# Performance work log

Hardware: AMD Instinct MI355X
Metric: run time of the kernel (lower is better)

Reference implementation:

```python
import jax, jax.numpy as jnp
import numpy as np

B, S, T = 32, 128, 64
V, E, H = 32000, 256, 512


def setup_inputs() -> dict:
    key = jax.random.key(0)
    ks = jax.random.split(key, 32)
    n = jax.random.normal

    def lin(k, fi, fo):
        kw, kb = jax.random.split(k)
        s = 1.0 / np.sqrt(fi)
        return (jax.random.uniform(kw, (fi, fo), jnp.float32, -s, s),
                jax.random.uniform(kb, (fo,), jnp.float32, -s, s))

    W_enc, b_enc = lin(ks[4], 2 * H, H)      # attention.enc_h_in
    W_prev, b_prev = lin(ks[5], H, H)        # attention.prev_s_in
    W_att, b_att = lin(ks[6], H, 1)          # attention.linear
    Wi_g, bi_g = lin(ks[7], E, 2 * H)        # cell.input_weights
    Wh_g, bh_g = lin(ks[8], H, 2 * H)        # cell.hidden_weights
    Wc_g, bc_g = lin(ks[9], 2 * H, 2 * H)    # cell.ctx_weights
    Wi, bi = lin(ks[10], E, H)               # cell.input_in
    Wh, bh = lin(ks[11], H, H)               # cell.hidden_in
    Wc, bc = lin(ks[12], 2 * H, H)           # cell.ctx_in
    W_out, b_out = lin(ks[13], H, V)         # dec2word

    return dict(
        content=n(ks[0], (B, H), jnp.float32),
        sentiment=n(ks[1], (B, H), jnp.float32),
        hiddens=n(ks[2], (B, S, 2 * H), jnp.float32),
        target=jax.random.randint(ks[3], (B, T), 0, V, jnp.int32),
        embed=n(ks[14], (V, E), jnp.float32) * 0.02,
        W_enc=W_enc, b_enc=b_enc, W_prev=W_prev, b_prev=b_prev,
        W_att=W_att, b_att=b_att,
        Wi_g=Wi_g, bi_g=bi_g, Wh_g=Wh_g, bh_g=bh_g, Wc_g=Wc_g, bc_g=bc_g,
        Wi=Wi, bi=bi, Wh=Wh, bh=bh, Wc=Wc, bc=bc,
        W_out=W_out, b_out=b_out,
    )


def reference(content, sentiment, hiddens, target, embed,
              W_enc, b_enc, W_prev, b_prev, W_att, b_att,
              Wi_g, bi_g, Wh_g, bh_g, Wc_g, bc_g,
              Wi, bi, Wh, bh, Wc, bc, W_out, b_out):
    tgt_emb = embed[target]                       # [B, T, E]
    enc_proj = hiddens @ W_enc + b_enc            # [B, S, H], timestep-invariant

    def step(prev_s, x_t):
        # additive attention
        q = prev_s @ W_prev + b_prev              # [B, H]
        h = jnp.tanh(enc_proj + q[:, None, :])    # [B, S, H]
        score = h @ W_att + b_att                 # [B, S, 1]
        alpha = jax.nn.softmax(score, axis=1)     # over source positions
        ctx = jnp.einsum('bsi,bsh->bh', alpha, hiddens)  # [B, 2H]
        # GRU-like cell (original uses only the first gate, as written)
        gates = x_t @ Wi_g + bi_g + prev_s @ Wh_g + bh_g + ctx @ Wc_g + bc_g
        reset_gate, _update_gate = jnp.split(gates, 2, axis=1)
        r = jax.nn.sigmoid(reset_gate)
        s_tilde = jnp.tanh(x_t @ Wi + bi + prev_s @ Wh + bh + ctx @ Wc + bc)
        new_s = (1.0 - r) * prev_s + r * s_tilde
        return new_s, new_s

    _, dec_h = jax.lax.scan(step, content, jnp.swapaxes(tgt_emb, 0, 1))
    dec_h = jnp.swapaxes(dec_h, 0, 1)             # [B, T, H]
    style_logits = sentiment @ W_out + b_out      # [B, V], same every step
    outputs = (dec_h @ W_out + b_out) + 0.5 * style_logits[:, None, :]
    return outputs                                # [B, T, V]
```

## Files before the change

kernel.cpp:

```cpp
#include <hip/hip_runtime.h>
#include <hip/hip_bf16.h>
#include <math.h>

#define NB 32
#define NS 128
#define NT 64
#define NV 32000
#define NE 256
#define NH 512

typedef short s16x8 __attribute__((ext_vector_type(8)));
typedef float f32x4 __attribute__((ext_vector_type(4)));
typedef unsigned u32x4 __attribute__((ext_vector_type(4)));

__device__ __forceinline__ unsigned short f2bf(float x) {
    union { float f; unsigned u; } v; v.f = x;
    unsigned r = v.u + 0x7FFFu + ((v.u >> 16) & 1u);
    return (unsigned short)(r >> 16);
}
__device__ __forceinline__ float bf2f(short h) {
    union { unsigned u; float f; } x;
    x.u = ((unsigned)(unsigned short)h) << 16;
    return x.f;
}

__device__ __forceinline__ void st_coh_b32(void* p, unsigned v) {
    asm volatile("global_store_dword %0, %1, off sc0 sc1" :: "v"(p), "v"(v) : "memory");
}
__device__ __forceinline__ unsigned ld_coh_b32(const void* p) {
    unsigned v;
    asm volatile("global_load_dword %0, %1, off sc0 sc1\n\ts_waitcnt vmcnt(0)"
                 : "=v"(v) : "v"(p) : "memory");
    return v;
}
__device__ __forceinline__ void ld_coh_2x128(const void* p0, const void* p1, u32x4& a, u32x4& b) {
    asm volatile("global_load_dwordx4 %0, %2, off sc0 sc1\n\t"
                 "global_load_dwordx4 %1, %3, off sc0 sc1\n\t"
                 "s_waitcnt vmcnt(0)"
                 : "=&v"(a), "=&v"(b) : "v"(p0), "v"(p1) : "memory");
}
__device__ __forceinline__ void ld_coh_3x32(const void* p0, const void* p1, const void* p2,
                                            float& a, float& b, float& c) {
    asm volatile("global_load_dword %0, %3, off sc0 sc1\n\t"
                 "global_load_dword %1, %4, off sc0 sc1\n\t"
                 "global_load_dword %2, %5, off sc0 sc1\n\t"
                 "s_waitcnt vmcnt(0)"
                 : "=&v"(a), "=&v"(b), "=&v"(c) : "v"(p0), "v"(p1), "v"(p2) : "memory");
}

__device__ __forceinline__ void wait_flags(const unsigned* flags, unsigned seq) {
    const int lane = threadIdx.x & 63;
    for (;;) {
        unsigned v = 0xFFFFFFFFu;
        if (lane < 32) v = ld_coh_b32(&flags[lane]);
        if (__all(v >= seq)) break;
    }
    asm volatile("" ::: "memory");
}

__global__ void build_wfrag_k(const float* __restrict__ Wp,
                              const float* __restrict__ Whg,
                              const float* __restrict__ Wh,
                              unsigned short* __restrict__ wfrag) {
    int blk = blockIdx.x;
    int lane = threadIdx.x;
    int ct = blk >> 4, kt = blk & 15;
    int c = ct * 16 + (lane & 15);
    int kb = kt * 32 + (lane >> 4) * 8;
    s16x8 v;
#pragma unroll
    for (int j = 0; j < 8; ++j) {
        int k = kb + j;
        float x;
        if (c < 512)       x = Wp[k * 512 + c];
        else if (c < 1024) x = Whg[k * 1024 + (c - 512)];
        else               x = Wh[k * 512 + (c - 1024)];
        v[j] = (short)f2bf(x);
    }
    ((s16x8*)wfrag)[blk * 64 + lane] = v;
}

template<int MODE>
__global__ __launch_bounds__(256, 2) void gemm_mfma(
    const float* __restrict__ Af, const unsigned short* __restrict__ Abf,
    const int* __restrict__ gidx,
    const float* __restrict__ B0, const float* __restrict__ B1, const float* __restrict__ B2,
    const float* __restrict__ e0, const float* __restrict__ e1, const float* __restrict__ e2,
    const float* __restrict__ e3, const float* __restrict__ e4, const float* __restrict__ e5,
    void* __restrict__ O0v, void* __restrict__ O1v, void* __restrict__ O2v)
{
    constexpr int M   = (MODE == 0) ? 4096 : 2048;
    constexpr int K   = (MODE == 0) ? 1024 : ((MODE == 1) ? 256 : 512);
    constexpr int LDA = (MODE == 0) ? 1024 : ((MODE == 1) ? 256 : 512);
    constexpr int MB  = M / 128;

    const int bm = blockIdx.x % MB, bn = blockIdx.x / MB;
    const int m0 = bm * 128, n0 = bn * 128;

    const float* Bp; int ldb, coff;
    if constexpr (MODE == 0) {
        int sub = n0 >> 9;
        Bp   = (sub == 0) ? B0 : (sub == 1) ? B1 : B2;
        ldb  = (sub == 1) ? 1024 : 512;
        coff = n0 & 511;
    } else if constexpr (MODE == 1) {
        if (n0 < 512) { Bp = B0; ldb = 1024; coff = n0; }
        else          { Bp = B1; ldb = 512;  coff = n0 - 512; }
    } else {
        Bp = B0; ldb = 32000; coff = n0;
    }

    __shared__ unsigned short As[128 * 40];
    __shared__ unsigned short Bs[128 * 40];

    const int tid = threadIdx.x, lane = tid & 63, w = tid >> 6;
    const int wr = w >> 1, wc = w & 1;
    const int k0f = (lane >> 4) * 8;
    const int rsel = lane & 15;

    f32x4 acc[4][4];
#pragma unroll
    for (int i = 0; i < 4; ++i)
#pragma unroll
        for (int j = 0; j < 4; ++j) { f32x4 z = {0.f, 0.f, 0.f, 0.f}; acc[i][j] = z; }

    for (int kt = 0; kt < K / 32; ++kt) {
        const int k0 = kt * 32;
        __syncthreads();
#pragma unroll
        for (int i = 0; i < 16; ++i) {
            int idx = tid + i * 256;
            int r = idx >> 5, k = idx & 31;
            unsigned short v;
            if constexpr (MODE == 2) {
                v = Abf[(size_t)(m0 + r) * LDA + k0 + k];
            } else if constexpr (MODE == 1) {
                int g = gidx[m0 + r];
                v = f2bf(Af[(size_t)g * 256 + k0 + k]);
            } else {
                v = f2bf(Af[(size_t)(m0 + r) * LDA + k0 + k]);
            }
            As[r * 40 + k] = v;
        }
#pragma unroll
        for (int i = 0; i < 16; ++i) {
            int idx = tid + i * 256;
            int k = idx >> 7, c = idx & 127;
            Bs[c * 40 + k] = f2bf(Bp[(size_t)(k0 + k) * ldb + coff + c]);
        }
        __syncthreads();

        s16x8 af[4], bf[4];
#pragma unroll
        for (int i = 0; i < 4; ++i)
            af[i] = *(const s16x8*)&As[(wr * 64 + i * 16 + rsel) * 40 + k0f];
#pragma unroll
        for (int j = 0; j < 4; ++j)
            bf[j] = *(const s16x8*)&Bs[(wc * 64 + j * 16 + rsel) * 40 + k0f];
#pragma unroll
        for (int i = 0; i < 4; ++i)
#pragma unroll
            for (int j = 0; j < 4; ++j)
                acc[i][j] = __builtin_amdgcn_mfma_f32_16x16x32_bf16(af[i], bf[j], acc[i][j], 0, 0, 0);
    }

    const int rg = (lane >> 4) * 4;
#pragma unroll
    for (int i = 0; i < 4; ++i)
#pragma unroll
        for (int j = 0; j < 4; ++j) {
            int row0 = m0 + wr * 64 + i * 16 + rg;
            int col  = n0 + wc * 64 + j * 16 + rsel;
            if constexpr (MODE == 0) {
                int sub = col >> 9;
                if (sub == 0) {
                    unsigned short* Ta = (unsigned short*)O0v;
#pragma unroll
                    for (int r = 0; r < 4; ++r)
                        Ta[(size_t)(row0 + r) * 512 + col] = f2bf(tanhf(acc[i][j][r] + e0[col]));
                } else {
                    int h = col & 511;
                    int bb = row0 >> 7, s0 = row0 & 127;
                    unsigned long long pk = 0;
#pragma unroll
                    for (int r = 0; r < 4; ++r)
                        pk |= (unsigned long long)f2bf(acc[i][j][r]) << (16 * r);
                    unsigned short* dstp = (sub == 1) ? (unsigned short*)O1v : (unsigned short*)O2v;
                    *(unsigned long long*)&dstp[(size_t)((bb * 512 + h) * 128 + s0)] = pk;
                }
            } else if constexpr (MODE == 1) {
                float* Of = (float*)O0v;
                float bias;
                if (col < 512) bias = e0[col] + e1[col] + e2[col];
                else { int h = col - 512; bias = e3[h] + e4[h] + e5[h]; }
#pragma unroll
                for (int r = 0; r < 4; ++r)
                    Of[(size_t)(row0 + r) * 1024 + col] = acc[i][j][r] + bias;
            } else {
                float* Of = (float*)O0v;
#pragma unroll
                for (int r = 0; r < 4; ++r)
                    Of[(size_t)(row0 + r) * 32000 + col] = acc[i][j][r] + 1.5f * e0[col];
            }
        }
}

__global__ __launch_bounds__(1024) void scan_coop(
    const float* __restrict__ content, const float* __restrict__ sentiment,
    const float* __restrict__ b_prev,  const float* __restrict__ W_att,
    const unsigned short* __restrict__ Ta_bf,
    const unsigned short* __restrict__ hWcg_t,
    const unsigned short* __restrict__ hWc_t,
    const float* __restrict__ xgxs, const unsigned short* __restrict__ wfrag,
    unsigned* __restrict__ S32, float* __restrict__ Ug,
    unsigned* __restrict__ flagS, unsigned* __restrict__ flagU,
    unsigned short* __restrict__ dh)
{
    const int b = blockIdx.x;
    const int tid = threadIdx.x, lane = tid & 63, w = tid >> 6;
    const unsigned long long* S64 = (const unsigned long long*)S32;

    __shared__ unsigned short W_lds[3 * 16 * 64 * 8];
    __shared__ unsigned short S_lds[32 * 536];
    __shared__ float tq[512];
    __shared__ float sc[128], al[128];
    __shared__ float cg[512], cs[512];

    {
        const s16x8* src = (const s16x8*)wfrag + (size_t)b * (3 * 16 * 64);
        s16x8* dst = (s16x8*)W_lds;
        for (int i = tid; i < 3 * 16 * 64; i += 1024) dst[i] = src[i];
    }
    float s_reg = 0.f, senth = 0.f, bprev_h = 0.f;
    if (tid < 512) {
        s_reg   = content[b * 512 + tid];
        senth   = 0.5f * sentiment[b * 512 + tid];
        bprev_h = b_prev[tid];
    }
    float wv[8];
    {
        const f32x4* wa = (const f32x4*)&W_att[lane * 8];
        f32x4 a0 = wa[0], a1 = wa[1];
#pragma unroll
        for (int j = 0; j < 4; ++j) { wv[j] = a0[j]; wv[4 + j] = a1[j]; }
    }
    const int kbase = (lane >> 4) * 8;

    if (tid < 512) {
        float nsn = __shfl_down(s_reg, 1, 64);
        if (!(lane & 1)) {
            unsigned p = (unsigned)f2bf(s_reg) | ((unsigned)f2bf(nsn) << 16);
            st_coh_b32(&S32[b * 256 + (tid >> 1)], p);
        }
    }
    asm volatile("s_waitcnt vmcnt(0)" ::: "memory");
    __syncthreads();
    if (tid == 0) st_coh_b32(&flagS[b], 1u);

    for (int t = 0; t < 64; ++t) {
        const size_t xrow = (size_t)b * 64 + t;
        float xg_pre = 0.f, xs_pre = 0.f;
        if (tid < 512) {
            xg_pre = xgxs[xrow * 1024 + tid];
            xs_pre = xgxs[xrow * 1024 + 512 + tid];
        }

        if (w == 15) wait_flags(flagS, (unsigned)(t + 1));
        __syncthreads();
        {
            int g0 = tid * 4;
            int r = g0 >> 7, so = (g0 & 127) * 4;
            u32x4 a, c;
            ld_coh_2x128(&S64[g0], &S64[g0 + 2], a, c);
            *(u32x4*)&S_lds[r * 536 + so]     = a;
            *(u32x4*)&S_lds[r * 536 + so + 8] = c;
        }
        __syncthreads();
        if (w < 6) {
            const int mt = w & 1, ct = w >> 1;
            const int arow = mt * 16 + (lane & 15);
            f32x4 ae = {0.f, 0.f, 0.f, 0.f}, ao = {0.f, 0.f, 0.f, 0.f};
            const s16x8* wl = (const s16x8*)W_lds;
#pragma unroll
            for (int kt = 0; kt < 16; kt += 2) {
                s16x8 a0 = *(const s16x8*)&S_lds[arow * 536 + kt * 32 + kbase];
                s16x8 a1 = *(const s16x8*)&S_lds[arow * 536 + (kt + 1) * 32 + kbase];
                ae = __builtin_amdgcn_mfma_f32_16x16x32_bf16(a0, wl[(ct * 16 + kt) * 64 + lane], ae, 0, 0, 0);
                ao = __builtin_amdgcn_mfma_f32_16x16x32_bf16(a1, wl[(ct * 16 + kt + 1) * 64 + lane], ao, 0, 0, 0);
            }
            f32x4 a4 = ae + ao;
            const int cout = b * 48 + ct * 16 + (lane & 15);
            const int rbase = mt * 16 + (lane >> 4) * 4;
#pragma unroll
            for (int r = 0; r < 4; ++r)
                st_coh_b32(&Ug[(rbase + r) * 1536 + cout], __float_as_uint(a4[r]));
            asm volatile("s_waitcnt vmcnt(0)" ::: "memory");
        }
        __syncthreads();
        if (tid == 0) st_coh_b32(&flagU[b], (unsigned)(t + 1));
        if (w == 15) wait_flags(flagU, (unsigned)(t + 1));
        __syncthreads();

        float guv = 0.f, suv = 0.f;
        if (tid < 512) {
            float qv;
            ld_coh_3x32(&Ug[b * 1536 + tid], &Ug[b * 1536 + 512 + tid],
                        &Ug[b * 1536 + 1024 + tid], qv, guv, suv);
            tq[tid] = tanhf(qv + bprev_h);
        }
        __syncthreads();
        {
            float tqv[8];
            const f32x4* tp = (const f32x4*)&tq[lane * 8];
            f32x4 t0 = tp[0], t1 = tp[1];
#pragma unroll
            for (int j = 0; j < 4; ++j) { tqv[j] = t0[j]; tqv[4 + j] = t1[j]; }
#pragma unroll
            for (int s8 = 0; s8 < 8; ++s8) {
                int s = w * 8 + s8;
                s16x8 tv = *(const s16x8*)&Ta_bf[((size_t)(b * 128 + s)) * 512 + lane * 8];
                float a = 0.f;
#pragma unroll
                for (int j = 0; j < 8; ++j) {
                    float ta = bf2f(tv[j]);
                    float num = ta + tqv[j];
                    float den = fmaf(ta, tqv[j], 1.0f);
                    a = fmaf(wv[j], num * __builtin_amdgcn_rcpf(den), a);
                }
#pragma unroll
                for (int off = 32; off; off >>= 1) a += __shfl_xor(a, off, 64);
                if (lane == 0) sc[s] = a;
            }
        }
        __syncthreads();
        if (w == 0) {
            float v0 = sc[lane], v1 = sc[lane + 64];
            float m = fmaxf(v0, v1);
#pragma unroll
            for (int off = 32; off; off >>= 1) m = fmaxf(m, __shfl_xor(m, off, 64));
            float p0 = __expf(v0 - m), p1 = __expf(v1 - m);
            float sm = p0 + p1;
#pragma unroll
            for (int off = 32; off; off >>= 1) sm += __shfl_xor(sm, off, 64);
            float inv = __builtin_amdgcn_rcpf(sm);
            al[lane] = p0 * inv; al[lane + 64] = p1 * inv;
        }
        __syncthreads();
        {
            int mat = tid >> 9, h = tid & 511;
            const s16x8* Mp = (const s16x8*)((mat ? hWc_t : hWcg_t) + ((size_t)(b * 512 + h)) * 128);
            float a0 = 0.f, a1 = 0.f;
#pragma unroll
            for (int q = 0; q < 16; ++q) {
                s16x8 v = Mp[q];
#pragma unroll
                for (int j = 0; j < 8; j += 2) {
                    a0 = fmaf(al[q * 8 + j],     bf2f(v[j]),     a0);
                    a1 = fmaf(al[q * 8 + j + 1], bf2f(v[j + 1]), a1);
                }
            }
            if (mat) cs[h] = a0 + a1; else cg[h] = a0 + a1;
        }
        __syncthreads();
        if (tid < 512) {
            int h = tid;
            float g  = guv + xg_pre + cg[h];
            float r  = __builtin_amdgcn_rcpf(1.0f + __expf(-g));
            float sp = suv + xs_pre + cs[h];
            float e  = __expf(2.0f * sp);
            float st = 1.0f - 2.0f * __builtin_amdgcn_rcpf(e + 1.0f);
            float ns = s_reg + r * (st - s_reg);
            s_reg = ns;
            dh[xrow * 512 + h] = f2bf(ns + senth);
            if (t < 63) {
                float nsn = __shfl_down(ns, 1, 64);
                if (!(lane & 1)) {
                    unsigned p = (unsigned)f2bf(ns) | ((unsigned)f2bf(nsn) << 16);
                    st_coh_b32(&S32[b * 256 + (h >> 1)], p);
                }
            }
        }
        asm volatile("s_waitcnt vmcnt(0)" ::: "memory");
        __syncthreads();
        if (t < 63 && tid == 0) st_coh_b32(&flagS[b], (unsigned)(t + 2));
    }
}

extern "C" void kernel_launch(void* const* d_in, const int* in_sizes, int n_in,
                              void* d_out, int out_size, void* d_ws, size_t ws_size,
                              hipStream_t stream) {
    const float* content  = (const float*)d_in[0];
    const float* sentiment= (const float*)d_in[1];
    const float* hiddens  = (const float*)d_in[2];
    const int*   target   = (const int*)  d_in[3];
    const float* embed    = (const float*)d_in[4];
    const float* W_enc = (const float*)d_in[5];  const float* b_enc = (const float*)d_in[6];
    const float* W_prev= (const float*)d_in[7];  const float* b_prev= (const float*)d_in[8];
    const float* W_att = (const float*)d_in[9];
    const float* Wi_g  = (const float*)d_in[11]; const float* bi_g  = (const float*)d_in[12];
    const float* Wh_g  = (const float*)d_in[13]; const float* bh_g  = (const float*)d_in[14];
    const float* Wc_g  = (const float*)d_in[15]; const float* bc_g  = (const float*)d_in[16];
    const float* Wi    = (const float*)d_in[17]; const float* bi    = (const float*)d_in[18];
    const float* Wh    = (const float*)d_in[19]; const float* bh    = (const float*)d_in[20];
    const float* Wc    = (const float*)d_in[21]; const float* bc    = (const float*)d_in[22];
    const float* W_out = (const float*)d_in[23]; const float* b_out = (const float*)d_in[24];
    float* out = (float*)d_out;

    char* ws = (char*)d_ws;
    unsigned short* wfrag = (unsigned short*)ws;
    unsigned* flagS = (unsigned*)(ws + 0x180000);
    unsigned* flagU = (unsigned*)(ws + 0x180100);
    float* Ug       = (float*)(ws + 0x181000);
    unsigned short* Ta_bf   = (unsigned short*)(ws + 0x1B1000);
    unsigned short* hWcg_t  = (unsigned short*)(ws + 0x5B1000);
    unsigned short* hWc_t   = (unsigned short*)(ws + 0x9B1000);
    float* xgxs     = (float*)(ws + 0xDB1000);
    unsigned short* dh      = (unsigned short*)(ws + 0x15B1000);
    unsigned* S32   = (unsigned*)(ws + 0x17B1000);

    hipMemsetAsync(ws + 0x180000, 0, 512, stream);

    build_wfrag_k<<<96 * 16, 64, 0, stream>>>(W_prev, Wh_g, Wh, wfrag);

    gemm_mfma<0><<<32 * 12, 256, 0, stream>>>(
        hiddens, nullptr, nullptr, W_enc, Wc_g, Wc,
        b_enc, nullptr, nullptr, nullptr, nullptr, nullptr,
        (void*)Ta_bf, (void*)hWcg_t, (void*)hWc_t);

    gemm_mfma<1><<<16 * 8, 256, 0, stream>>>(
        embed, nullptr, target, Wi_g, Wi, nullptr,
        bi_g, bh_g, bc_g, bi, bh, bc,
        (void*)xgxs, nullptr, nullptr);

    scan_coop<<<NB, 1024, 0, stream>>>(
        content, sentiment, b_prev, W_att, Ta_bf, hWcg_t, hWc_t,
        xgxs, wfrag, S32, Ug, flagS, flagU, dh);

    gemm_mfma<2><<<16 * 250, 256, 0, stream>>>(
        nullptr, dh, nullptr, W_out, nullptr, nullptr,
        b_out, nullptr, nullptr, nullptr, nullptr, nullptr,
        (void*)out, nullptr, nullptr);

    (void)in_sizes; (void)n_in; (void)out_size; (void)ws_size;
}
```

Measured before the change: 1.452 ms.

## Replace flag-based grid barriers with per-element tagged payloads in recurrent scan

The cooperative scan kernel used to publish the state and the projection results, then raise per-block flags that other blocks polled, with block-wide syncs and store drains around each exchange. Now every 32-bit value is stored together with a step tag in a 64-bit word, and consumers poll the data directly until every tag matches the current step. This drops the separate flag round-trips and several __syncthreads per timestep from the serial critical path. In exchange, the exchanged buffers double in size, every thread spins on global loads, and correctness depends on each 64-bit store being observed atomically.

```diff
diff --git a/kernel.cpp b/kernel.cpp
--- a/kernel.cpp
+++ b/kernel.cpp
@@ -11,7 +11,6 @@
 
 typedef short s16x8 __attribute__((ext_vector_type(8)));
 typedef float f32x4 __attribute__((ext_vector_type(4)));
-typedef unsigned u32x4 __attribute__((ext_vector_type(4)));
 
 __device__ __forceinline__ unsigned short f2bf(float x) {
     union { float f; unsigned u; } v; v.f = x;
@@ -24,38 +23,43 @@
     return x.f;
 }
 
-__device__ __forceinline__ void st_coh_b32(void* p, unsigned v) {
-    asm volatile("global_store_dword %0, %1, off sc0 sc1" :: "v"(p), "v"(v) : "memory");
-}
-__device__ __forceinline__ unsigned ld_coh_b32(const void* p) {
-    unsigned v;
-    asm volatile("global_load_dword %0, %1, off sc0 sc1\n\ts_waitcnt vmcnt(0)"
-                 : "=v"(v) : "v"(p) : "memory");
-    return v;
-}
-__device__ __forceinline__ void ld_coh_2x128(const void* p0, const void* p1, u32x4& a, u32x4& b) {
-    asm volatile("global_load_dwordx4 %0, %2, off sc0 sc1\n\t"
-                 "global_load_dwordx4 %1, %3, off sc0 sc1\n\t"
-                 "s_waitcnt vmcnt(0)"
-                 : "=&v"(a), "=&v"(b) : "v"(p0), "v"(p1) : "memory");
-}
-__device__ __forceinline__ void ld_coh_3x32(const void* p0, const void* p1, const void* p2,
-                                            float& a, float& b, float& c) {
-    asm volatile("global_load_dword %0, %3, off sc0 sc1\n\t"
-                 "global_load_dword %1, %4, off sc0 sc1\n\t"
-                 "global_load_dword %2, %5, off sc0 sc1\n\t"
-                 "s_waitcnt vmcnt(0)"
-                 : "=&v"(a), "=&v"(b), "=&v"(c) : "v"(p0), "v"(p1), "v"(p2) : "memory");
-}
-
-__device__ __forceinline__ void wait_flags(const unsigned* flags, unsigned seq) {
-    const int lane = threadIdx.x & 63;
-    for (;;) {
-        unsigned v = 0xFFFFFFFFu;
-        if (lane < 32) v = ld_coh_b32(&flags[lane]);
-        if (__all(v >= seq)) break;
-    }
-    asm volatile("" ::: "memory");
+__device__ __forceinline__ void st_pt(unsigned long long* p, unsigned pay, unsigned tag) {
+    unsigned long long v = (unsigned long long)pay | ((unsigned long long)tag << 32);
+    asm volatile("global_store_dwordx2 %0, %1, off sc0 sc1" :: "v"(p), "v"(v) : "memory");
+}
+__device__ __forceinline__ void ld8_pt(const unsigned long long* b0, unsigned long long* v) {
+    unsigned long long v0, v1, v2, v3, v4, v5, v6, v7;
+    asm volatile(
+        "global_load_dwordx2 %0, %8, off sc0 sc1\n\t"
+        "global_load_dwordx2 %1, %9, off sc0 sc1\n\t"
+        "global_load_dwordx2 %2, %10, off sc0 sc1\n\t"
+        "global_load_dwordx2 %3, %11, off sc0 sc1\n\t"
+        "global_load_dwordx2 %4, %12, off sc0 sc1\n\t"
+        "global_load_dwordx2 %5, %13, off sc0 sc1\n\t"
+        "global_load_dwordx2 %6, %14, off sc0 sc1\n\t"
+        "global_load_dwordx2 %7, %15, off sc0 sc1\n\t"
+        "s_waitcnt vmcnt(0)"
+        : "=&v"(v0), "=&v"(v1), "=&v"(v2), "=&v"(v3),
+          "=&v"(v4), "=&v"(v5), "=&v"(v6), "=&v"(v7)
+        : "v"(b0), "v"(b0 + 1024), "v"(b0 + 2048), "v"(b0 + 3072),
+          "v"(b0 + 4096), "v"(b0 + 5120), "v"(b0 + 6144), "v"(b0 + 7168)
+        : "memory");
+    v[0] = v0; v[1] = v1; v[2] = v2; v[3] = v3;
+    v[4] = v4; v[5] = v5; v[6] = v6; v[7] = v7;
+}
+__device__ __forceinline__ void ld3_pt(const unsigned long long* p0,
+                                       const unsigned long long* p1,
+                                       const unsigned long long* p2,
+                                       unsigned long long& a, unsigned long long& b,
+                                       unsigned long long& c) {
+    asm volatile(
+        "global_load_dwordx2 %0, %3, off sc0 sc1\n\t"
+        "global_load_dwordx2 %1, %4, off sc0 sc1\n\t"
+        "global_load_dwordx2 %2, %5, off sc0 sc1\n\t"
+        "s_waitcnt vmcnt(0)"
+        : "=&v"(a), "=&v"(b), "=&v"(c)
+        : "v"(p0), "v"(p1), "v"(p2)
+        : "memory");
 }
 
 __global__ void build_wfrag_k(const float* __restrict__ Wp,
@@ -205,20 +209,18 @@
         }
 }
 
-__global__ __launch_bounds__(1024) void scan_coop(
+__global__ __launch_bounds__(1024) void scan_df(
     const float* __restrict__ content, const float* __restrict__ sentiment,
     const float* __restrict__ b_prev,  const float* __restrict__ W_att,
     const unsigned short* __restrict__ Ta_bf,
     const unsigned short* __restrict__ hWcg_t,
     const unsigned short* __restrict__ hWc_t,
     const float* __restrict__ xgxs, const unsigned short* __restrict__ wfrag,
-    unsigned* __restrict__ S32, float* __restrict__ Ug,
-    unsigned* __restrict__ flagS, unsigned* __restrict__ flagU,
+    unsigned long long* __restrict__ Spl, unsigned long long* __restrict__ Upl,
     unsigned short* __restrict__ dh)
 {
     const int b = blockIdx.x;
     const int tid = threadIdx.x, lane = tid & 63, w = tid >> 6;
-    const unsigned long long* S64 = (const unsigned long long*)S32;
 
     __shared__ unsigned short W_lds[3 * 16 * 64 * 8];
     __shared__ unsigned short S_lds[32 * 536];
@@ -249,15 +251,13 @@
     if (tid < 512) {
         float nsn = __shfl_down(s_reg, 1, 64);
         if (!(lane & 1)) {
-            unsigned p = (unsigned)f2bf(s_reg) | ((unsigned)f2bf(nsn) << 16);
-            st_coh_b32(&S32[b * 256 + (tid >> 1)], p);
-        }
-    }
-    asm volatile("s_waitcnt vmcnt(0)" ::: "memory");
-    __syncthreads();
-    if (tid == 0) st_coh_b32(&flagS[b], 1u);
+            unsigned pay = (unsigned)f2bf(s_reg) | ((unsigned)f2bf(nsn) << 16);
+            st_pt(&Spl[b * 256 + (tid >> 1)], pay, 1u);
+        }
+    }
 
     for (int t = 0; t < 64; ++t) {
+        const unsigned want = (unsigned)(t + 1);
         const size_t xrow = (size_t)b * 64 + t;
         float xg_pre = 0.f, xs_pre = 0.f;
         if (tid < 512) {
@@ -265,17 +265,26 @@
             xs_pre = xgxs[xrow * 1024 + 512 + tid];
         }
 
-        if (w == 15) wait_flags(flagS, (unsigned)(t + 1));
-        __syncthreads();
         {
-            int g0 = tid * 4;
-            int r = g0 >> 7, so = (g0 & 127) * 4;
-            u32x4 a, c;
-            ld_coh_2x128(&S64[g0], &S64[g0 + 2], a, c);
-            *(u32x4*)&S_lds[r * 536 + so]     = a;
-            *(u32x4*)&S_lds[r * 536 + so + 8] = c;
-        }
-        __syncthreads();
+            unsigned long long v[8];
+            const unsigned long long* base = &Spl[tid];
+            ld8_pt(base, v);
+            for (;;) {
+                bool ok = true;
+#pragma unroll
+                for (int ii = 0; ii < 8; ++ii) ok &= ((unsigned)(v[ii] >> 32) == want);
+                if (ok) break;
+                ld8_pt(base, v);
+            }
+#pragma unroll
+            for (int ii = 0; ii < 8; ++ii) {
+                int idx = tid + ii * 1024;
+                int r = idx >> 8, c = (idx & 255) * 2;
+                *(unsigned*)&S_lds[r * 536 + c] = (unsigned)v[ii];
+            }
+        }
+        __syncthreads();
+
         if (w < 6) {
             const int mt = w & 1, ct = w >> 1;
             const int arow = mt * 16 + (lane & 15);
@@ -293,22 +302,27 @@
             const int rbase = mt * 16 + (lane >> 4) * 4;
 #pragma unroll
             for (int r = 0; r < 4; ++r)
-                st_coh_b32(&Ug[(rbase + r) * 1536 + cout], __float_as_uint(a4[r]));
-            asm volatile("s_waitcnt vmcnt(0)" ::: "memory");
-        }
-        __syncthreads();
-        if (tid == 0) st_coh_b32(&flagU[b], (unsigned)(t + 1));
-        if (w == 15) wait_flags(flagU, (unsigned)(t + 1));
-        __syncthreads();
+                st_pt(&Upl[(size_t)(rbase + r) * 1536 + cout], __float_as_uint(a4[r]), want);
+        }
 
         float guv = 0.f, suv = 0.f;
         if (tid < 512) {
-            float qv;
-            ld_coh_3x32(&Ug[b * 1536 + tid], &Ug[b * 1536 + 512 + tid],
-                        &Ug[b * 1536 + 1024 + tid], qv, guv, suv);
+            unsigned long long u0, u1, u2;
+            const unsigned long long* q0 = &Upl[b * 1536 + tid];
+            const unsigned long long* q1 = &Upl[b * 1536 + 512 + tid];
+            const unsigned long long* q2 = &Upl[b * 1536 + 1024 + tid];
+            ld3_pt(q0, q1, q2, u0, u1, u2);
+            while (((unsigned)(u0 >> 32) != want) | ((unsigned)(u1 >> 32) != want) |
+                   ((unsigned)(u2 >> 32) != want)) {
+                ld3_pt(q0, q1, q2, u0, u1, u2);
+            }
+            float qv = __uint_as_float((unsigned)u0);
+            guv = __uint_as_float((unsigned)u1);
+            suv = __uint_as_float((unsigned)u2);
             tq[tid] = tanhf(qv + bprev_h);
         }
         __syncthreads();
+
         {
             float tqv[8];
             const f32x4* tp = (const f32x4*)&tq[lane * 8];
@@ -375,14 +389,12 @@
             if (t < 63) {
                 float nsn = __shfl_down(ns, 1, 64);
                 if (!(lane & 1)) {
-                    unsigned p = (unsigned)f2bf(ns) | ((unsigned)f2bf(nsn) << 16);
-                    st_coh_b32(&S32[b * 256 + (h >> 1)], p);
+                    unsigned pay = (unsigned)f2bf(ns) | ((unsigned)f2bf(nsn) << 16);
+                    st_pt(&Spl[b * 256 + (h >> 1)], pay, (unsigned)(t + 2));
                 }
             }
         }
-        asm volatile("s_waitcnt vmcnt(0)" ::: "memory");
-        __syncthreads();
-        if (t < 63 && tid == 0) st_coh_b32(&flagS[b], (unsigned)(t + 2));
+        __syncthreads();
     }
 }
 
@@ -408,17 +420,15 @@
 
     char* ws = (char*)d_ws;
     unsigned short* wfrag = (unsigned short*)ws;
-    unsigned* flagS = (unsigned*)(ws + 0x180000);
-    unsigned* flagU = (unsigned*)(ws + 0x180100);
-    float* Ug       = (float*)(ws + 0x181000);
-    unsigned short* Ta_bf   = (unsigned short*)(ws + 0x1B1000);
-    unsigned short* hWcg_t  = (unsigned short*)(ws + 0x5B1000);
-    unsigned short* hWc_t   = (unsigned short*)(ws + 0x9B1000);
-    float* xgxs     = (float*)(ws + 0xDB1000);
-    unsigned short* dh      = (unsigned short*)(ws + 0x15B1000);
-    unsigned* S32   = (unsigned*)(ws + 0x17B1000);
-
-    hipMemsetAsync(ws + 0x180000, 0, 512, stream);
+    unsigned long long* Spl = (unsigned long long*)(ws + 0x180000);
+    unsigned long long* Upl = (unsigned long long*)(ws + 0x190000);
+    unsigned short* Ta_bf   = (unsigned short*)(ws + 0x200000);
+    unsigned short* hWcg_t  = (unsigned short*)(ws + 0x600000);
+    unsigned short* hWc_t   = (unsigned short*)(ws + 0xA00000);
+    float* xgxs     = (float*)(ws + 0xE00000);
+    unsigned short* dh      = (unsigned short*)(ws + 0x1600000);
+
+    hipMemsetAsync(ws + 0x180000, 0, 0x70000, stream);
 
     build_wfrag_k<<<96 * 16, 64, 0, stream>>>(W_prev, Wh_g, Wh, wfrag);
 
@@ -432,9 +442,9 @@
         bi_g, bh_g, bc_g, bi, bh, bc,
         (void*)xgxs, nullptr, nullptr);
 
-    scan_coop<<<NB, 1024, 0, stream>>>(
+    scan_df<<<NB, 1024, 0, stream>>>(
         content, sentiment, b_prev, W_att, Ta_bf, hWcg_t, hWc_t,
-        xgxs, wfrag, S32, Ug, flagS, flagU, dh);
+        xgxs, wfrag, Spl, Upl, dh);
 
     gemm_mfma<2><<<16 * 250, 256, 0, stream>>>(
         nullptr, dh, nullptr, W_out, nullptr, nullptr,
```

Result: faster. 1.369 ms (-5.7%).
